# Kernel optimization log

Measured on AMD Instinct MI355X. Metric: run time of the kernel, lower is better.

The kernel has to match this reference:

```python
import jax, jax.numpy as jnp
import numpy as np

N = 50000      # nodes
E = 800000     # message edges
P = 200000     # prediction edges
C_IN = 64      # in_channels
C_H = 64       # hidden_channels


def setup_inputs() -> dict:
    key = jax.random.key(0)
    ks = jax.random.split(key, 20)
    s = 0.05
    inp = {
        "x": jax.random.normal(ks[0], (N, C_IN), jnp.float32),
        "prediction_edges": jax.random.randint(ks[1], (2, P), 0, N, dtype=jnp.int32),
        "message_edges": jax.random.randint(ks[2], (2, E), 0, N, dtype=jnp.int32),
        "message_edgewt": jax.random.uniform(ks[3], (E,), jnp.float32),
        # conv1 params
        "coef1": jnp.float32(0.5),
        "pool1_w": jax.random.normal(ks[4], (C_IN, C_IN), jnp.float32) * s,
        "pool1_b": jnp.zeros((C_IN,), jnp.float32),
        "fin1_w": jax.random.normal(ks[5], (C_H, 2 * C_IN), jnp.float32) * s,
        "fin1_b": jnp.zeros((C_H,), jnp.float32),
        # conv2 params
        "coef2": jnp.float32(0.5),
        "pool2_w": jax.random.normal(ks[6], (C_H, C_H), jnp.float32) * s,
        "pool2_b": jnp.zeros((C_H,), jnp.float32),
        "fin2_w": jax.random.normal(ks[7], (C_H, 2 * C_H), jnp.float32) * s,
        "fin2_b": jnp.zeros((C_H,), jnp.float32),
        # edge heads
        "ewp_w": jax.random.normal(ks[8], (1, 2 * C_H), jnp.float32) * s,
        "ewp_b": jnp.zeros((1,), jnp.float32),
        "ep_w": jax.random.normal(ks[9], (1, 2 * C_H), jnp.float32) * s,
        "ep_b": jnp.zeros((1,), jnp.float32),
    }
    return inp


def _relu(v):
    return jnp.maximum(v, 0)


def _sage_conv(x, src, dst, ew, coef, pw, pb, fw, fb):
    n = x.shape[0]
    all_src = jnp.concatenate([src, dst])   # [2E]
    all_dst = jnp.concatenate([dst, src])   # [2E]
    neigh = x[all_src]                       # [2E, C] gather
    w2 = jnp.concatenate([ew, ew])           # [2E]
    edge_feat = neigh * (1.0 + coef * w2[:, None])
    pooled = _relu(edge_feat @ pw.T + pb)    # [2E, C]
    # self-loop edges (src == dst) routed to dummy segment n
    seg = jnp.where(all_src != all_dst, all_dst, n)
    agg = jax.ops.segment_max(pooled, seg, num_segments=n + 1)[:n]
    agg = jnp.where(jnp.isfinite(agg), agg, 0.0)  # empty nodes -> 0
    h = jnp.concatenate([x, agg], axis=-1)   # [N, 2C]
    return _relu(h @ fw.T + fb)


def reference(x, prediction_edges, message_edges, message_edgewt,
              coef1, pool1_w, pool1_b, fin1_w, fin1_b,
              coef2, pool2_w, pool2_b, fin2_w, fin2_b,
              ewp_w, ewp_b, ep_w, ep_b):
    src, dst = message_edges[0], message_edges[1]
    h = _sage_conv(x, src, dst, message_edgewt, coef1, pool1_w, pool1_b, fin1_w, fin1_b)
    h = _sage_conv(h, src, dst, message_edgewt, coef2, pool2_w, pool2_b, fin2_w, fin2_b)
    emb = jnp.concatenate([h[prediction_edges[0]], h[prediction_edges[1]]], axis=-1)  # [P, 2C]
    edge_weights = _relu(emb @ ewp_w.T + ewp_b)   # [P, 1]
    edge_predictor = emb @ ep_w.T + ep_b          # [P, 1]
    return edge_weights, edge_predictor
```

## Files before the change

### kernel.cpp

```cpp
#include <hip/hip_runtime.h>


typedef _Float16 h16;
typedef __attribute__((ext_vector_type(4))) _Float16 h16x4;
typedef __attribute__((ext_vector_type(4))) float f32x4;
#define MFMA16(a, b, c) __builtin_amdgcn_mfma_f32_16x16x16f16(a, b, c, 0, 0, 0)

#define NBMAX 1600
#define NFB   128

__global__ void cvt_kernel(const float* __restrict__ X,
                           h16* __restrict__ X16, int n8) {
    int t = blockIdx.x * blockDim.x + threadIdx.x;
    const int stride = gridDim.x * blockDim.x;
    for (int i = t; i < n8; i += stride) {
        const float4 a = ((const float4*)X)[2 * i];
        const float4 b = ((const float4*)X)[2 * i + 1];
        h16x4 lo = {(h16)a.x, (h16)a.y, (h16)a.z, (h16)a.w};
        h16x4 hi = {(h16)b.x, (h16)b.y, (h16)b.z, (h16)b.w};
        ((h16x4*)X16)[2 * i] = lo;
        ((h16x4*)X16)[2 * i + 1] = hi;
    }
}

__global__ __launch_bounds__(256, 2)
void mmA_kernel(const h16* __restrict__ X16, const float* __restrict__ W,
                h16* __restrict__ Z, int ntiles) {
    const int lane = threadIdx.x & 63;
    const int c = lane & 15, q = lane >> 4;
    int wave = (int)((blockIdx.x * blockDim.x + threadIdx.x) >> 6);
    const int nwaves = (int)((gridDim.x * blockDim.x) >> 6);
    h16x4 bf[4][4];
#pragma unroll
    for (int ct = 0; ct < 4; ++ct)
#pragma unroll
        for (int ks = 0; ks < 4; ++ks) {
            const float4 w4 = *(const float4*)(W + (ct * 16 + c) * 64 + ks * 16 + q * 4);
            bf[ct][ks] = (h16x4){(h16)w4.x, (h16)w4.y, (h16)w4.z, (h16)w4.w};
        }
    for (int t = wave; t < ntiles; t += nwaves) {
        const int n0 = t * 16;
        const h16* __restrict__ xrow = X16 + (size_t)(n0 + c) * 64 + q * 4;
        h16x4 af[4];
#pragma unroll
        for (int ks = 0; ks < 4; ++ks) af[ks] = *(const h16x4*)(xrow + ks * 16);
        f32x4 acc[4];
#pragma unroll
        for (int ct = 0; ct < 4; ++ct) acc[ct] = (f32x4){0.f, 0.f, 0.f, 0.f};
#pragma unroll
        for (int ct = 0; ct < 4; ++ct)
#pragma unroll
            for (int ks = 0; ks < 4; ++ks)
                acc[ct] = MFMA16(af[ks], bf[ct][ks], acc[ct]);
#pragma unroll
        for (int ct = 0; ct < 4; ++ct)
#pragma unroll
            for (int m = 0; m < 4; ++m)
                Z[(size_t)(n0 + q * 4 + m) * 64 + ct * 16 + c] = (h16)acc[ct][m];
    }
}

__global__ __launch_bounds__(256, 2)
void finA_kernel(const h16* __restrict__ XA, const h16* __restrict__ XB,
                 const float* __restrict__ W, const float* __restrict__ b,
                 h16* __restrict__ H, int ntiles) {
    const int lane = threadIdx.x & 63;
    const int c = lane & 15, q = lane >> 4;
    int wave = (int)((blockIdx.x * blockDim.x + threadIdx.x) >> 6);
    const int nwaves = (int)((gridDim.x * blockDim.x) >> 6);
    h16x4 bf[4][8];
#pragma unroll
    for (int ct = 0; ct < 4; ++ct)
#pragma unroll
        for (int ks = 0; ks < 8; ++ks) {
            const float4 w4 = *(const float4*)(W + (ct * 16 + c) * 128 + ks * 16 + q * 4);
            bf[ct][ks] = (h16x4){(h16)w4.x, (h16)w4.y, (h16)w4.z, (h16)w4.w};
        }
    float bc[4];
#pragma unroll
    for (int ct = 0; ct < 4; ++ct) bc[ct] = b[ct * 16 + c];
    for (int t = wave; t < ntiles; t += nwaves) {
        const int n0 = t * 16;
        const h16* __restrict__ ra = XA + (size_t)(n0 + c) * 64 + q * 4;
        const h16* __restrict__ rb = XB + (size_t)(n0 + c) * 64 + q * 4;
        h16x4 af[8];
#pragma unroll
        for (int ks = 0; ks < 4; ++ks) {
            af[ks] = *(const h16x4*)(ra + ks * 16);
            af[4 + ks] = *(const h16x4*)(rb + ks * 16);
        }
        f32x4 acc[4];
#pragma unroll
        for (int ct = 0; ct < 4; ++ct) acc[ct] = (f32x4){bc[ct], bc[ct], bc[ct], bc[ct]};
#pragma unroll
        for (int ct = 0; ct < 4; ++ct)
#pragma unroll
            for (int ks = 0; ks < 8; ++ks)
                acc[ct] = MFMA16(af[ks], bf[ct][ks], acc[ct]);
#pragma unroll
        for (int ct = 0; ct < 4; ++ct)
#pragma unroll
            for (int m = 0; m < 4; ++m)
                H[(size_t)(n0 + q * 4 + m) * 64 + ct * 16 + c] =
                    (h16)fmaxf(acc[ct][m], 0.f);
    }
}

__global__ __launch_bounds__(256, 2)
void fin2A_kernel(const h16* __restrict__ XA, const h16* __restrict__ XB,
                  const float* __restrict__ W, const float* __restrict__ b,
                  const float* __restrict__ ewp_w, const float* __restrict__ ep_w,
                  float4* __restrict__ nodeheads, int ntiles) {
    const int lane = threadIdx.x & 63;
    const int c = lane & 15, q = lane >> 4;
    int wave = (int)((blockIdx.x * blockDim.x + threadIdx.x) >> 6);
    const int nwaves = (int)((gridDim.x * blockDim.x) >> 6);
    h16x4 bf[4][8];
#pragma unroll
    for (int ct = 0; ct < 4; ++ct)
#pragma unroll
        for (int ks = 0; ks < 8; ++ks) {
            const float4 w4 = *(const float4*)(W + (ct * 16 + c) * 128 + ks * 16 + q * 4);
            bf[ct][ks] = (h16x4){(h16)w4.x, (h16)w4.y, (h16)w4.z, (h16)w4.w};
        }
    float bc[4], hw1s[4], hw1d[4], hw2s[4], hw2d[4];
#pragma unroll
    for (int ct = 0; ct < 4; ++ct) {
        bc[ct] = b[ct * 16 + c];
        hw1s[ct] = ewp_w[ct * 16 + c];
        hw1d[ct] = ewp_w[64 + ct * 16 + c];
        hw2s[ct] = ep_w[ct * 16 + c];
        hw2d[ct] = ep_w[64 + ct * 16 + c];
    }
    for (int t = wave; t < ntiles; t += nwaves) {
        const int n0 = t * 16;
        const h16* __restrict__ ra = XA + (size_t)(n0 + c) * 64 + q * 4;
        const h16* __restrict__ rb = XB + (size_t)(n0 + c) * 64 + q * 4;
        h16x4 af[8];
#pragma unroll
        for (int ks = 0; ks < 4; ++ks) {
            af[ks] = *(const h16x4*)(ra + ks * 16);
            af[4 + ks] = *(const h16x4*)(rb + ks * 16);
        }
        f32x4 acc[4];
#pragma unroll
        for (int ct = 0; ct < 4; ++ct) acc[ct] = (f32x4){bc[ct], bc[ct], bc[ct], bc[ct]};
#pragma unroll
        for (int ct = 0; ct < 4; ++ct)
#pragma unroll
            for (int ks = 0; ks < 8; ++ks)
                acc[ct] = MFMA16(af[ks], bf[ct][ks], acc[ct]);
        f32x4 r1 = {0.f, 0.f, 0.f, 0.f}, r2 = r1, r3 = r1, r4 = r1;
#pragma unroll
        for (int ct = 0; ct < 4; ++ct)
#pragma unroll
            for (int m = 0; m < 4; ++m) {
                const float h = fmaxf(acc[ct][m], 0.f);
                r1[m] = fmaf(hw1s[ct], h, r1[m]);
                r2[m] = fmaf(hw1d[ct], h, r2[m]);
                r3[m] = fmaf(hw2s[ct], h, r3[m]);
                r4[m] = fmaf(hw2d[ct], h, r4[m]);
            }
#pragma unroll
        for (int off = 1; off < 16; off <<= 1)
#pragma unroll
            for (int m = 0; m < 4; ++m) {
                r1[m] += __shfl_xor(r1[m], off, 16);
                r2[m] += __shfl_xor(r2[m], off, 16);
                r3[m] += __shfl_xor(r3[m], off, 16);
                r4[m] += __shfl_xor(r4[m], off, 16);
            }
        if (c == 0) {
#pragma unroll
            for (int m = 0; m < 4; ++m)
                nodeheads[n0 + q * 4 + m] =
                    make_float4(r1[m], r2[m], r3[m], r4[m]);
        }
    }
}

__global__ void hist_kernel(const int* __restrict__ esrc,
                            const int* __restrict__ edst,
                            int* __restrict__ bucketTotal,
                            int* __restrict__ blockBase, int E, int NB) {
    __shared__ int cnt[NBMAX];
    for (int b = threadIdx.x; b < NB; b += blockDim.x) cnt[b] = 0;
    __syncthreads();
    const int chunk = (E + gridDim.x - 1) / gridDim.x;
    const int start = blockIdx.x * chunk;
    const int end = min(start + chunk, E);
    for (int e = start + (int)threadIdx.x; e < end; e += blockDim.x) {
        const int s = esrc[e];
        const int d = edst[e];
        if (s != d) {
            atomicAdd(&cnt[d >> 5], 1);
            atomicAdd(&cnt[s >> 5], 1);
        }
    }
    __syncthreads();
    for (int b = threadIdx.x; b < NB; b += blockDim.x)
        blockBase[(size_t)blockIdx.x * NB + b] = atomicAdd(&bucketTotal[b], cnt[b]);
}

__global__ void scan_kernel(const int* __restrict__ deg,
                            int* __restrict__ offs, int n) {
    __shared__ int wsum[16];
    __shared__ int s_carry;
    const int tid = threadIdx.x;
    const int lane = tid & 63;
    const int wid = tid >> 6;
    if (tid == 0) s_carry = 0;
    __syncthreads();
    for (int base = 0; base < n; base += 1024) {
        const int i = base + tid;
        const int v = (i < n) ? deg[i] : 0;
        int x = v;
#pragma unroll
        for (int off = 1; off < 64; off <<= 1) {
            int t = __shfl_up(x, off, 64);
            if (lane >= off) x += t;
        }
        if (lane == 63) wsum[wid] = x;
        __syncthreads();
        if (wid == 0) {
            int wv = (lane < 16) ? wsum[lane] : 0;
#pragma unroll
            for (int off = 1; off < 16; off <<= 1) {
                int t = __shfl_up(wv, off, 64);
                if (lane >= off) wv += t;
            }
            if (lane < 16) wsum[lane] = wv;
        }
        __syncthreads();
        const int carry = s_carry;
        const int waveoff = (wid > 0) ? wsum[wid - 1] : 0;
        if (i < n) offs[i] = carry + waveoff + x - v;
        __syncthreads();
        if (tid == 0) s_carry = carry + wsum[15];
        __syncthreads();
    }
}

__global__ void binfill_kernel(const int* __restrict__ esrc,
                               const int* __restrict__ edst,
                               const float* __restrict__ ewt,
                               const int* __restrict__ bucketStart,
                               const int* __restrict__ blockBase,
                               unsigned* __restrict__ entries, int E, int NB) {
    __shared__ int cur[NBMAX];
    for (int b = threadIdx.x; b < NB; b += blockDim.x)
        cur[b] = bucketStart[b] + blockBase[(size_t)blockIdx.x * NB + b];
    __syncthreads();
    const int chunk = (E + gridDim.x - 1) / gridDim.x;
    const int start = blockIdx.x * chunk;
    const int end = min(start + chunk, E);
    for (int e = start + (int)threadIdx.x; e < end; e += blockDim.x) {
        const int s = esrc[e];
        const int d = edst[e];
        if (s != d) {
            const unsigned wq =
                (unsigned)fminf(ewt[e] * 2048.f + 0.5f, 2047.f) << 21;
            const int pd = atomicAdd(&cur[d >> 5], 1);
            entries[pd] = (unsigned)s | ((unsigned)(d & 31) << 16) | wq;
            const int ps = atomicAdd(&cur[s >> 5], 1);
            entries[ps] = (unsigned)d | ((unsigned)(s & 31) << 16) | wq;
        }
    }
}

__global__ void sortbucket_kernel(const int* __restrict__ bucketStart,
                                  const int* __restrict__ bucketTotal,
                                  const unsigned* __restrict__ in,
                                  unsigned* __restrict__ out,
                                  int* __restrict__ nodeBeg, int n, int NB) {
    __shared__ int bin[32];
    __shared__ int cur[32];
    const int bkt = blockIdx.x;
    const int beg = bucketStart[bkt];
    const int cnt = bucketTotal[bkt];
    if (threadIdx.x < 32) bin[threadIdx.x] = 0;
    __syncthreads();
    for (int i = threadIdx.x; i < cnt; i += blockDim.x)
        atomicAdd(&bin[(in[beg + i] >> 16) & 31u], 1);
    __syncthreads();
    if (threadIdx.x == 0) {
        int run = 0;
#pragma unroll
        for (int r = 0; r < 32; ++r) { cur[r] = run; run += bin[r]; }
    }
    __syncthreads();
    if (threadIdx.x < 32) {
        const int node = bkt * 32 + (int)threadIdx.x;
        if (node < n) nodeBeg[node] = beg + cur[threadIdx.x];
    }
    if (bkt == NB - 1 && threadIdx.x == 0) nodeBeg[n] = beg + cnt;
    __syncthreads();
    for (int i = threadIdx.x; i < cnt; i += blockDim.x) {
        const unsigned e = in[beg + i];
        const int pos = beg + atomicAdd(&cur[(e >> 16) & 31u], 1);
        out[pos] = e;
    }
}

__global__ void aggregateN_kernel(const int* __restrict__ nodeBeg,
                                  const unsigned* __restrict__ entries,
                                  const h16* __restrict__ Z,
                                  const float* __restrict__ pb,
                                  const float* __restrict__ coefp,
                                  h16* __restrict__ agg, int n) {
    const int lane = threadIdx.x & 63;
    int wave = (int)((blockIdx.x * blockDim.x + threadIdx.x) >> 6);
    const int nwaves = (int)((gridDim.x * blockDim.x) >> 6);
    const float coefq = coefp[0] * (1.f / 2048.f);
    const float pbc = pb[lane];
    for (int d = wave; d < n; d += nwaves) {
        const int du = __builtin_amdgcn_readfirstlane(d);
        const int beg = nodeBeg[du];
        const int end = nodeBeg[du + 1];
        float m0 = 0.f, m1 = 0.f, m2 = 0.f, m3 = 0.f;
        int i = beg;
        for (; i + 4 <= end; i += 4) {
            const unsigned e0 = (unsigned)__builtin_amdgcn_readfirstlane((int)entries[i]);
            const unsigned e1 = (unsigned)__builtin_amdgcn_readfirstlane((int)entries[i + 1]);
            const unsigned e2 = (unsigned)__builtin_amdgcn_readfirstlane((int)entries[i + 2]);
            const unsigned e3 = (unsigned)__builtin_amdgcn_readfirstlane((int)entries[i + 3]);
            const float z0 = (float)Z[(size_t)(e0 & 0xffffu) * 64 + lane];
            const float z1 = (float)Z[(size_t)(e1 & 0xffffu) * 64 + lane];
            const float z2 = (float)Z[(size_t)(e2 & 0xffffu) * 64 + lane];
            const float z3 = (float)Z[(size_t)(e3 & 0xffffu) * 64 + lane];
            m0 = fmaxf(m0, fmaf(fmaf(coefq, (float)(e0 >> 21), 1.f), z0, pbc));
            m1 = fmaxf(m1, fmaf(fmaf(coefq, (float)(e1 >> 21), 1.f), z1, pbc));
            m2 = fmaxf(m2, fmaf(fmaf(coefq, (float)(e2 >> 21), 1.f), z2, pbc));
            m3 = fmaxf(m3, fmaf(fmaf(coefq, (float)(e3 >> 21), 1.f), z3, pbc));
        }
        for (; i < end; ++i) {
            const unsigned e = (unsigned)__builtin_amdgcn_readfirstlane((int)entries[i]);
            const float zv = (float)Z[(size_t)(e & 0xffffu) * 64 + lane];
            m0 = fmaxf(m0, fmaf(fmaf(coefq, (float)(e >> 21), 1.f), zv, pbc));
        }
        agg[(size_t)du * 64 + lane] = (h16)fmaxf(fmaxf(m0, m1), fmaxf(m2, m3));
    }
}

__global__ void headsP_kernel(const int* __restrict__ psrc,
                              const int* __restrict__ pdst,
                              const float4* __restrict__ nodeheads,
                              const float* __restrict__ ewp_b,
                              const float* __restrict__ ep_b,
                              float* __restrict__ out, int P) {
    int t = blockIdx.x * blockDim.x + threadIdx.x;
    const int stride = gridDim.x * blockDim.x;
    const float b1 = ewp_b[0], b2 = ep_b[0];
    for (; t < P; t += stride) {
        const float4 qs = nodeheads[psrc[t]];
        const float4 qd = nodeheads[pdst[t]];
        out[t] = fmaxf(qs.x + qd.y + b1, 0.f);
        out[(size_t)P + t] = qs.z + qd.w + b2;
    }
}

extern "C" void kernel_launch(void* const* d_in, const int* in_sizes, int n_in,
                              void* d_out, int out_size, void* d_ws, size_t ws_size,
                              hipStream_t stream) {
    const float* x      = (const float*)d_in[0];
    const int*   pe     = (const int*)d_in[1];
    const int*   me     = (const int*)d_in[2];
    const float* mew    = (const float*)d_in[3];
    const float* coef1  = (const float*)d_in[4];
    const float* p1w    = (const float*)d_in[5];
    const float* p1b    = (const float*)d_in[6];
    const float* f1w    = (const float*)d_in[7];
    const float* f1b    = (const float*)d_in[8];
    const float* coef2  = (const float*)d_in[9];
    const float* p2w    = (const float*)d_in[10];
    const float* p2b    = (const float*)d_in[11];
    const float* f2w    = (const float*)d_in[12];
    const float* f2b    = (const float*)d_in[13];
    const float* ewp_w  = (const float*)d_in[14];
    const float* ewp_b  = (const float*)d_in[15];
    const float* ep_w   = (const float*)d_in[16];
    const float* ep_b   = (const float*)d_in[17];

    const int n = in_sizes[0] / 64;
    const int P = in_sizes[1] / 2;
    const int E = in_sizes[2] / 2;
    const int NB = (n + 31) >> 5;
    const int ntiles = (n + 15) >> 4;

    float4* nodeheads = (float4*)d_ws;
    h16* z16   = (h16*)(nodeheads + n);
    h16* agg16 = z16 + (size_t)n * 64;
    h16* h1    = agg16 + (size_t)n * 64;
    h16* x16   = h1 + (size_t)n * 64;
    unsigned* entriesA = (unsigned*)(x16 + (size_t)n * 64);
    unsigned* entriesB = entriesA + 2 * (size_t)E;
    int* bucketTotal = (int*)(entriesB + 2 * (size_t)E);
    int* bucketStart = bucketTotal + NBMAX;
    int* nodeBeg     = bucketStart + NBMAX;
    int* blockBase   = nodeBeg + (n + 1);

    const int* esrc = me;
    const int* edst = me + E;
    const int* psrc = pe;
    const int* pdst = pe + P;

    const dim3 blk(256);
    const int mfGrid = (ntiles + 3) / 4;
    const int agGrid = 2048;
    const int hpGrid = (P + 255) / 256;

    cvt_kernel<<<1024, blk, 0, stream>>>(x, x16, n * 64 / 8);
    hipMemsetAsync(bucketTotal, 0, (size_t)NB * sizeof(int), stream);
    hist_kernel<<<NFB, blk, 0, stream>>>(esrc, edst, bucketTotal, blockBase, E, NB);
    scan_kernel<<<1, 1024, 0, stream>>>(bucketTotal, bucketStart, NB);
    binfill_kernel<<<NFB, blk, 0, stream>>>(esrc, edst, mew, bucketStart,
                                            blockBase, entriesA, E, NB);
    sortbucket_kernel<<<NB, blk, 0, stream>>>(bucketStart, bucketTotal,
                                              entriesA, entriesB, nodeBeg, n, NB);

    mmA_kernel<<<mfGrid, blk, 0, stream>>>(x16, p1w, z16, ntiles);
    aggregateN_kernel<<<agGrid, blk, 0, stream>>>(nodeBeg, entriesB, z16,
                                                  p1b, coef1, agg16, n);
    finA_kernel<<<mfGrid, blk, 0, stream>>>(x16, agg16, f1w, f1b, h1, ntiles);

    mmA_kernel<<<mfGrid, blk, 0, stream>>>(h1, p2w, z16, ntiles);
    aggregateN_kernel<<<agGrid, blk, 0, stream>>>(nodeBeg, entriesB, z16,
                                                  p2b, coef2, agg16, n);
    fin2A_kernel<<<mfGrid, blk, 0, stream>>>(h1, agg16, f2w, f2b,
                                             ewp_w, ep_w, nodeheads, ntiles);

    headsP_kernel<<<hpGrid, blk, 0, stream>>>(psrc, pdst, nodeheads,
                                              ewp_b, ep_b, (float*)d_out, P);
}
```

Baseline: 206.7 us.

## Fuse graph build into cooperative kernel and aggregation with final linear

Merges the histogram, scan, bin-fill and bucket-sort kernels into one cooperative kernel separated by grid syncs. It also fuses neighbour max-aggregation with the final linear layer per 32-node group, staging aggregates in LDS instead of writing them to global memory. The fp32-to-fp16 conversion pass is folded into the first matmul. The aim is fewer launches and less intermediate memory traffic, at the cost of grid-sync overhead and a fixed 32-node block granularity for aggregation.

```diff
diff --git a/kernel.cpp b/kernel.cpp
--- a/kernel.cpp
+++ b/kernel.cpp
@@ -1,4 +1,7 @@
 #include <hip/hip_runtime.h>
+#include <hip/hip_cooperative_groups.h>
+
+namespace cg = cooperative_groups;
 
 
 typedef _Float16 h16;
@@ -7,183 +10,25 @@
 #define MFMA16(a, b, c) __builtin_amdgcn_mfma_f32_16x16x16f16(a, b, c, 0, 0, 0)
 
 #define NBMAX 1600
-#define NFB   128
-
-__global__ void cvt_kernel(const float* __restrict__ X,
-                           h16* __restrict__ X16, int n8) {
-    int t = blockIdx.x * blockDim.x + threadIdx.x;
-    const int stride = gridDim.x * blockDim.x;
-    for (int i = t; i < n8; i += stride) {
-        const float4 a = ((const float4*)X)[2 * i];
-        const float4 b = ((const float4*)X)[2 * i + 1];
-        h16x4 lo = {(h16)a.x, (h16)a.y, (h16)a.z, (h16)a.w};
-        h16x4 hi = {(h16)b.x, (h16)b.y, (h16)b.z, (h16)b.w};
-        ((h16x4*)X16)[2 * i] = lo;
-        ((h16x4*)X16)[2 * i + 1] = hi;
-    }
-}
-
-__global__ __launch_bounds__(256, 2)
-void mmA_kernel(const h16* __restrict__ X16, const float* __restrict__ W,
-                h16* __restrict__ Z, int ntiles) {
-    const int lane = threadIdx.x & 63;
-    const int c = lane & 15, q = lane >> 4;
-    int wave = (int)((blockIdx.x * blockDim.x + threadIdx.x) >> 6);
-    const int nwaves = (int)((gridDim.x * blockDim.x) >> 6);
-    h16x4 bf[4][4];
-#pragma unroll
-    for (int ct = 0; ct < 4; ++ct)
-#pragma unroll
-        for (int ks = 0; ks < 4; ++ks) {
-            const float4 w4 = *(const float4*)(W + (ct * 16 + c) * 64 + ks * 16 + q * 4);
-            bf[ct][ks] = (h16x4){(h16)w4.x, (h16)w4.y, (h16)w4.z, (h16)w4.w};
-        }
-    for (int t = wave; t < ntiles; t += nwaves) {
-        const int n0 = t * 16;
-        const h16* __restrict__ xrow = X16 + (size_t)(n0 + c) * 64 + q * 4;
-        h16x4 af[4];
-#pragma unroll
-        for (int ks = 0; ks < 4; ++ks) af[ks] = *(const h16x4*)(xrow + ks * 16);
-        f32x4 acc[4];
-#pragma unroll
-        for (int ct = 0; ct < 4; ++ct) acc[ct] = (f32x4){0.f, 0.f, 0.f, 0.f};
-#pragma unroll
-        for (int ct = 0; ct < 4; ++ct)
-#pragma unroll
-            for (int ks = 0; ks < 4; ++ks)
-                acc[ct] = MFMA16(af[ks], bf[ct][ks], acc[ct]);
-#pragma unroll
-        for (int ct = 0; ct < 4; ++ct)
-#pragma unroll
-            for (int m = 0; m < 4; ++m)
-                Z[(size_t)(n0 + q * 4 + m) * 64 + ct * 16 + c] = (h16)acc[ct][m];
-    }
-}
-
-__global__ __launch_bounds__(256, 2)
-void finA_kernel(const h16* __restrict__ XA, const h16* __restrict__ XB,
-                 const float* __restrict__ W, const float* __restrict__ b,
-                 h16* __restrict__ H, int ntiles) {
-    const int lane = threadIdx.x & 63;
-    const int c = lane & 15, q = lane >> 4;
-    int wave = (int)((blockIdx.x * blockDim.x + threadIdx.x) >> 6);
-    const int nwaves = (int)((gridDim.x * blockDim.x) >> 6);
-    h16x4 bf[4][8];
-#pragma unroll
-    for (int ct = 0; ct < 4; ++ct)
-#pragma unroll
-        for (int ks = 0; ks < 8; ++ks) {
-            const float4 w4 = *(const float4*)(W + (ct * 16 + c) * 128 + ks * 16 + q * 4);
-            bf[ct][ks] = (h16x4){(h16)w4.x, (h16)w4.y, (h16)w4.z, (h16)w4.w};
-        }
-    float bc[4];
-#pragma unroll
-    for (int ct = 0; ct < 4; ++ct) bc[ct] = b[ct * 16 + c];
-    for (int t = wave; t < ntiles; t += nwaves) {
-        const int n0 = t * 16;
-        const h16* __restrict__ ra = XA + (size_t)(n0 + c) * 64 + q * 4;
-        const h16* __restrict__ rb = XB + (size_t)(n0 + c) * 64 + q * 4;
-        h16x4 af[8];
-#pragma unroll
-        for (int ks = 0; ks < 4; ++ks) {
-            af[ks] = *(const h16x4*)(ra + ks * 16);
-            af[4 + ks] = *(const h16x4*)(rb + ks * 16);
-        }
-        f32x4 acc[4];
-#pragma unroll
-        for (int ct = 0; ct < 4; ++ct) acc[ct] = (f32x4){bc[ct], bc[ct], bc[ct], bc[ct]};
-#pragma unroll
-        for (int ct = 0; ct < 4; ++ct)
-#pragma unroll
-            for (int ks = 0; ks < 8; ++ks)
-                acc[ct] = MFMA16(af[ks], bf[ct][ks], acc[ct]);
-#pragma unroll
-        for (int ct = 0; ct < 4; ++ct)
-#pragma unroll
-            for (int m = 0; m < 4; ++m)
-                H[(size_t)(n0 + q * 4 + m) * 64 + ct * 16 + c] =
-                    (h16)fmaxf(acc[ct][m], 0.f);
-    }
-}
-
-__global__ __launch_bounds__(256, 2)
-void fin2A_kernel(const h16* __restrict__ XA, const h16* __restrict__ XB,
-                  const float* __restrict__ W, const float* __restrict__ b,
-                  const float* __restrict__ ewp_w, const float* __restrict__ ep_w,
-                  float4* __restrict__ nodeheads, int ntiles) {
-    const int lane = threadIdx.x & 63;
-    const int c = lane & 15, q = lane >> 4;
-    int wave = (int)((blockIdx.x * blockDim.x + threadIdx.x) >> 6);
-    const int nwaves = (int)((gridDim.x * blockDim.x) >> 6);
-    h16x4 bf[4][8];
-#pragma unroll
-    for (int ct = 0; ct < 4; ++ct)
-#pragma unroll
-        for (int ks = 0; ks < 8; ++ks) {
-            const float4 w4 = *(const float4*)(W + (ct * 16 + c) * 128 + ks * 16 + q * 4);
-            bf[ct][ks] = (h16x4){(h16)w4.x, (h16)w4.y, (h16)w4.z, (h16)w4.w};
-        }
-    float bc[4], hw1s[4], hw1d[4], hw2s[4], hw2d[4];
-#pragma unroll
-    for (int ct = 0; ct < 4; ++ct) {
-        bc[ct] = b[ct * 16 + c];
-        hw1s[ct] = ewp_w[ct * 16 + c];
-        hw1d[ct] = ewp_w[64 + ct * 16 + c];
-        hw2s[ct] = ep_w[ct * 16 + c];
-        hw2d[ct] = ep_w[64 + ct * 16 + c];
-    }
-    for (int t = wave; t < ntiles; t += nwaves) {
-        const int n0 = t * 16;
-        const h16* __restrict__ ra = XA + (size_t)(n0 + c) * 64 + q * 4;
-        const h16* __restrict__ rb = XB + (size_t)(n0 + c) * 64 + q * 4;
-        h16x4 af[8];
-#pragma unroll
-        for (int ks = 0; ks < 4; ++ks) {
-            af[ks] = *(const h16x4*)(ra + ks * 16);
-            af[4 + ks] = *(const h16x4*)(rb + ks * 16);
-        }
-        f32x4 acc[4];
-#pragma unroll
-        for (int ct = 0; ct < 4; ++ct) acc[ct] = (f32x4){bc[ct], bc[ct], bc[ct], bc[ct]};
-#pragma unroll
-        for (int ct = 0; ct < 4; ++ct)
-#pragma unroll
-            for (int ks = 0; ks < 8; ++ks)
-                acc[ct] = MFMA16(af[ks], bf[ct][ks], acc[ct]);
-        f32x4 r1 = {0.f, 0.f, 0.f, 0.f}, r2 = r1, r3 = r1, r4 = r1;
-#pragma unroll
-        for (int ct = 0; ct < 4; ++ct)
-#pragma unroll
-            for (int m = 0; m < 4; ++m) {
-                const float h = fmaxf(acc[ct][m], 0.f);
-                r1[m] = fmaf(hw1s[ct], h, r1[m]);
-                r2[m] = fmaf(hw1d[ct], h, r2[m]);
-                r3[m] = fmaf(hw2s[ct], h, r3[m]);
-                r4[m] = fmaf(hw2d[ct], h, r4[m]);
-            }
-#pragma unroll
-        for (int off = 1; off < 16; off <<= 1)
-#pragma unroll
-            for (int m = 0; m < 4; ++m) {
-                r1[m] += __shfl_xor(r1[m], off, 16);
-                r2[m] += __shfl_xor(r2[m], off, 16);
-                r3[m] += __shfl_xor(r3[m], off, 16);
-                r4[m] += __shfl_xor(r4[m], off, 16);
-            }
-        if (c == 0) {
-#pragma unroll
-            for (int m = 0; m < 4; ++m)
-                nodeheads[n0 + q * 4 + m] =
-                    make_float4(r1[m], r2[m], r3[m], r4[m]);
-        }
-    }
-}
-
-__global__ void hist_kernel(const int* __restrict__ esrc,
-                            const int* __restrict__ edst,
-                            int* __restrict__ bucketTotal,
-                            int* __restrict__ blockBase, int E, int NB) {
+#define NFBC  256
+
+__global__ void coopbuild_kernel(const int* __restrict__ esrc,
+                                 const int* __restrict__ edst,
+                                 const float* __restrict__ ewt,
+                                 int* __restrict__ bucketTotal,
+                                 int* __restrict__ bucketStart,
+                                 int* __restrict__ blockBase,
+                                 unsigned* __restrict__ entriesA,
+                                 unsigned* __restrict__ entriesB,
+                                 int* __restrict__ nodeBeg,
+                                 int E, int NB, int n) {
+    cg::grid_group grid = cg::this_grid();
     __shared__ int cnt[NBMAX];
+    __shared__ int wsum[4];
+    __shared__ int s_carry;
+    __shared__ int bin[32];
+    __shared__ int cur32[32];
+
     for (int b = threadIdx.x; b < NB; b += blockDim.x) cnt[b] = 0;
     __syncthreads();
     const int chunk = (E + gridDim.x - 1) / gridDim.x;
@@ -200,145 +45,300 @@
     __syncthreads();
     for (int b = threadIdx.x; b < NB; b += blockDim.x)
         blockBase[(size_t)blockIdx.x * NB + b] = atomicAdd(&bucketTotal[b], cnt[b]);
-}
-
-__global__ void scan_kernel(const int* __restrict__ deg,
-                            int* __restrict__ offs, int n) {
-    __shared__ int wsum[16];
-    __shared__ int s_carry;
-    const int tid = threadIdx.x;
-    const int lane = tid & 63;
-    const int wid = tid >> 6;
-    if (tid == 0) s_carry = 0;
+    grid.sync();
+
+    if (blockIdx.x == 0) {
+        const int tid = threadIdx.x;
+        const int lane = tid & 63;
+        const int wid = tid >> 6;
+        if (tid == 0) s_carry = 0;
+        __syncthreads();
+        for (int base = 0; base < NB; base += blockDim.x) {
+            const int i = base + tid;
+            const int v = (i < NB) ? bucketTotal[i] : 0;
+            int x = v;
+#pragma unroll
+            for (int off = 1; off < 64; off <<= 1) {
+                int t = __shfl_up(x, off, 64);
+                if (lane >= off) x += t;
+            }
+            if (lane == 63) wsum[wid] = x;
+            __syncthreads();
+            if (wid == 0 && lane < 4) {
+                int wv = wsum[lane];
+#pragma unroll
+                for (int off = 1; off < 4; off <<= 1) {
+                    int t = __shfl_up(wv, off, 64);
+                    if (lane >= off) wv += t;
+                }
+                wsum[lane] = wv;
+            }
+            __syncthreads();
+            const int carry = s_carry;
+            const int waveoff = (wid > 0) ? wsum[wid - 1] : 0;
+            if (i < NB) bucketStart[i] = carry + waveoff + x - v;
+            __syncthreads();
+            if (tid == 0) s_carry = carry + wsum[3];
+            __syncthreads();
+        }
+    }
+    grid.sync();
+
+    for (int b = threadIdx.x; b < NB; b += blockDim.x)
+        cnt[b] = bucketStart[b] + blockBase[(size_t)blockIdx.x * NB + b];
     __syncthreads();
-    for (int base = 0; base < n; base += 1024) {
-        const int i = base + tid;
-        const int v = (i < n) ? deg[i] : 0;
-        int x = v;
-#pragma unroll
-        for (int off = 1; off < 64; off <<= 1) {
-            int t = __shfl_up(x, off, 64);
-            if (lane >= off) x += t;
-        }
-        if (lane == 63) wsum[wid] = x;
-        __syncthreads();
-        if (wid == 0) {
-            int wv = (lane < 16) ? wsum[lane] : 0;
-#pragma unroll
-            for (int off = 1; off < 16; off <<= 1) {
-                int t = __shfl_up(wv, off, 64);
-                if (lane >= off) wv += t;
-            }
-            if (lane < 16) wsum[lane] = wv;
-        }
-        __syncthreads();
-        const int carry = s_carry;
-        const int waveoff = (wid > 0) ? wsum[wid - 1] : 0;
-        if (i < n) offs[i] = carry + waveoff + x - v;
-        __syncthreads();
-        if (tid == 0) s_carry = carry + wsum[15];
-        __syncthreads();
-    }
-}
-
-__global__ void binfill_kernel(const int* __restrict__ esrc,
-                               const int* __restrict__ edst,
-                               const float* __restrict__ ewt,
-                               const int* __restrict__ bucketStart,
-                               const int* __restrict__ blockBase,
-                               unsigned* __restrict__ entries, int E, int NB) {
-    __shared__ int cur[NBMAX];
-    for (int b = threadIdx.x; b < NB; b += blockDim.x)
-        cur[b] = bucketStart[b] + blockBase[(size_t)blockIdx.x * NB + b];
-    __syncthreads();
-    const int chunk = (E + gridDim.x - 1) / gridDim.x;
-    const int start = blockIdx.x * chunk;
-    const int end = min(start + chunk, E);
     for (int e = start + (int)threadIdx.x; e < end; e += blockDim.x) {
         const int s = esrc[e];
         const int d = edst[e];
         if (s != d) {
             const unsigned wq =
                 (unsigned)fminf(ewt[e] * 2048.f + 0.5f, 2047.f) << 21;
-            const int pd = atomicAdd(&cur[d >> 5], 1);
-            entries[pd] = (unsigned)s | ((unsigned)(d & 31) << 16) | wq;
-            const int ps = atomicAdd(&cur[s >> 5], 1);
-            entries[ps] = (unsigned)d | ((unsigned)(s & 31) << 16) | wq;
-        }
+            const int pd = atomicAdd(&cnt[d >> 5], 1);
+            entriesA[pd] = (unsigned)s | ((unsigned)(d & 31) << 16) | wq;
+            const int ps = atomicAdd(&cnt[s >> 5], 1);
+            entriesA[ps] = (unsigned)d | ((unsigned)(s & 31) << 16) | wq;
+        }
+    }
+    grid.sync();
+
+    for (int bkt = blockIdx.x; bkt < NB; bkt += gridDim.x) {
+        const int beg = bucketStart[bkt];
+        const int cn = bucketTotal[bkt];
+        if (threadIdx.x < 32) bin[threadIdx.x] = 0;
+        __syncthreads();
+        for (int i = threadIdx.x; i < cn; i += blockDim.x)
+            atomicAdd(&bin[(entriesA[beg + i] >> 16) & 31u], 1);
+        __syncthreads();
+        if (threadIdx.x == 0) {
+            int run = 0;
+#pragma unroll
+            for (int r = 0; r < 32; ++r) { cur32[r] = run; run += bin[r]; }
+        }
+        __syncthreads();
+        if (threadIdx.x < 32) {
+            const int node = bkt * 32 + (int)threadIdx.x;
+            if (node < n) nodeBeg[node] = beg + cur32[threadIdx.x];
+        }
+        if (bkt == NB - 1 && threadIdx.x == 0) nodeBeg[n] = beg + cn;
+        __syncthreads();
+        for (int i = threadIdx.x; i < cn; i += blockDim.x) {
+            const unsigned e = entriesA[beg + i];
+            const int pos = beg + atomicAdd(&cur32[(e >> 16) & 31u], 1);
+            entriesB[pos] = e;
+        }
+        __syncthreads();
     }
 }
 
-__global__ void sortbucket_kernel(const int* __restrict__ bucketStart,
-                                  const int* __restrict__ bucketTotal,
-                                  const unsigned* __restrict__ in,
-                                  unsigned* __restrict__ out,
-                                  int* __restrict__ nodeBeg, int n, int NB) {
-    __shared__ int bin[32];
-    __shared__ int cur[32];
-    const int bkt = blockIdx.x;
-    const int beg = bucketStart[bkt];
-    const int cnt = bucketTotal[bkt];
-    if (threadIdx.x < 32) bin[threadIdx.x] = 0;
-    __syncthreads();
-    for (int i = threadIdx.x; i < cnt; i += blockDim.x)
-        atomicAdd(&bin[(in[beg + i] >> 16) & 31u], 1);
-    __syncthreads();
-    if (threadIdx.x == 0) {
-        int run = 0;
-#pragma unroll
-        for (int r = 0; r < 32; ++r) { cur[r] = run; run += bin[r]; }
-    }
-    __syncthreads();
-    if (threadIdx.x < 32) {
-        const int node = bkt * 32 + (int)threadIdx.x;
-        if (node < n) nodeBeg[node] = beg + cur[threadIdx.x];
-    }
-    if (bkt == NB - 1 && threadIdx.x == 0) nodeBeg[n] = beg + cnt;
-    __syncthreads();
-    for (int i = threadIdx.x; i < cnt; i += blockDim.x) {
-        const unsigned e = in[beg + i];
-        const int pos = beg + atomicAdd(&cur[(e >> 16) & 31u], 1);
-        out[pos] = e;
-    }
-}
-
-__global__ void aggregateN_kernel(const int* __restrict__ nodeBeg,
-                                  const unsigned* __restrict__ entries,
-                                  const h16* __restrict__ Z,
-                                  const float* __restrict__ pb,
-                                  const float* __restrict__ coefp,
-                                  h16* __restrict__ agg, int n) {
+template <bool XFP32>
+__global__ __launch_bounds__(256, 2)
+void mmA_kernel(const void* __restrict__ Xv, const float* __restrict__ W,
+                h16* __restrict__ Z, int ntiles) {
     const int lane = threadIdx.x & 63;
+    const int c = lane & 15, q = lane >> 4;
     int wave = (int)((blockIdx.x * blockDim.x + threadIdx.x) >> 6);
     const int nwaves = (int)((gridDim.x * blockDim.x) >> 6);
-    const float coefq = coefp[0] * (1.f / 2048.f);
-    const float pbc = pb[lane];
-    for (int d = wave; d < n; d += nwaves) {
-        const int du = __builtin_amdgcn_readfirstlane(d);
-        const int beg = nodeBeg[du];
-        const int end = nodeBeg[du + 1];
-        float m0 = 0.f, m1 = 0.f, m2 = 0.f, m3 = 0.f;
-        int i = beg;
-        for (; i + 4 <= end; i += 4) {
-            const unsigned e0 = (unsigned)__builtin_amdgcn_readfirstlane((int)entries[i]);
-            const unsigned e1 = (unsigned)__builtin_amdgcn_readfirstlane((int)entries[i + 1]);
-            const unsigned e2 = (unsigned)__builtin_amdgcn_readfirstlane((int)entries[i + 2]);
-            const unsigned e3 = (unsigned)__builtin_amdgcn_readfirstlane((int)entries[i + 3]);
-            const float z0 = (float)Z[(size_t)(e0 & 0xffffu) * 64 + lane];
-            const float z1 = (float)Z[(size_t)(e1 & 0xffffu) * 64 + lane];
-            const float z2 = (float)Z[(size_t)(e2 & 0xffffu) * 64 + lane];
-            const float z3 = (float)Z[(size_t)(e3 & 0xffffu) * 64 + lane];
-            m0 = fmaxf(m0, fmaf(fmaf(coefq, (float)(e0 >> 21), 1.f), z0, pbc));
-            m1 = fmaxf(m1, fmaf(fmaf(coefq, (float)(e1 >> 21), 1.f), z1, pbc));
-            m2 = fmaxf(m2, fmaf(fmaf(coefq, (float)(e2 >> 21), 1.f), z2, pbc));
-            m3 = fmaxf(m3, fmaf(fmaf(coefq, (float)(e3 >> 21), 1.f), z3, pbc));
-        }
-        for (; i < end; ++i) {
-            const unsigned e = (unsigned)__builtin_amdgcn_readfirstlane((int)entries[i]);
-            const float zv = (float)Z[(size_t)(e & 0xffffu) * 64 + lane];
-            m0 = fmaxf(m0, fmaf(fmaf(coefq, (float)(e >> 21), 1.f), zv, pbc));
-        }
-        agg[(size_t)du * 64 + lane] = (h16)fmaxf(fmaxf(m0, m1), fmaxf(m2, m3));
+    h16x4 bf[4][4];
+#pragma unroll
+    for (int ct = 0; ct < 4; ++ct)
+#pragma unroll
+        for (int ks = 0; ks < 4; ++ks) {
+            const float4 w4 = *(const float4*)(W + (ct * 16 + c) * 64 + ks * 16 + q * 4);
+            bf[ct][ks] = (h16x4){(h16)w4.x, (h16)w4.y, (h16)w4.z, (h16)w4.w};
+        }
+    for (int t = wave; t < ntiles; t += nwaves) {
+        const int n0 = t * 16;
+        h16x4 af[4];
+        if constexpr (XFP32) {
+            const float* xr = (const float*)Xv + (size_t)(n0 + c) * 64 + q * 4;
+#pragma unroll
+            for (int ks = 0; ks < 4; ++ks) {
+                const float4 v = *(const float4*)(xr + ks * 16);
+                af[ks] = (h16x4){(h16)v.x, (h16)v.y, (h16)v.z, (h16)v.w};
+            }
+        } else {
+            const h16* xr = (const h16*)Xv + (size_t)(n0 + c) * 64 + q * 4;
+#pragma unroll
+            for (int ks = 0; ks < 4; ++ks) af[ks] = *(const h16x4*)(xr + ks * 16);
+        }
+        f32x4 acc[4];
+#pragma unroll
+        for (int ct = 0; ct < 4; ++ct) acc[ct] = (f32x4){0.f, 0.f, 0.f, 0.f};
+#pragma unroll
+        for (int ct = 0; ct < 4; ++ct)
+#pragma unroll
+            for (int ks = 0; ks < 4; ++ks)
+                acc[ct] = MFMA16(af[ks], bf[ct][ks], acc[ct]);
+#pragma unroll
+        for (int ct = 0; ct < 4; ++ct)
+#pragma unroll
+            for (int m = 0; m < 4; ++m)
+                Z[(size_t)(n0 + q * 4 + m) * 64 + ct * 16 + c] = (h16)acc[ct][m];
+    }
+}
+
+template <bool XFP32, bool HEADS>
+__global__ __launch_bounds__(256, 2)
+void aggfin_kernel(const int* __restrict__ nodeBeg,
+                   const unsigned* __restrict__ entries,
+                   const h16* __restrict__ Z,
+                   const float* __restrict__ pb,
+                   const float* __restrict__ coefp,
+                   const void* __restrict__ Xv,
+                   const float* __restrict__ W,
+                   const float* __restrict__ bvec,
+                   const float* __restrict__ ewp_w,
+                   const float* __restrict__ ep_w,
+                   h16* __restrict__ H,
+                   float4* __restrict__ nodeheads,
+                   int n) {
+    __shared__ h16 ldsA[32 * 64];
+    __shared__ float4 ldsR[2][16][2];
+    const int lane = threadIdx.x & 63;
+    const int wid = threadIdx.x >> 6;
+    const int g0 = blockIdx.x * 32;
+
+    {
+        const float coefq = coefp[0] * (1.f / 2048.f);
+        const float pbc = pb[lane];
+        for (int ln = wid; ln < 32; ln += 4) {
+            const int node = g0 + ln;
+            float m0 = 0.f, m1 = 0.f, m2 = 0.f, m3 = 0.f;
+            if (node < n) {
+                const int beg = nodeBeg[node];
+                const int end = nodeBeg[node + 1];
+                int i = beg;
+                for (; i + 4 <= end; i += 4) {
+                    const unsigned e0 = (unsigned)__builtin_amdgcn_readfirstlane((int)entries[i]);
+                    const unsigned e1 = (unsigned)__builtin_amdgcn_readfirstlane((int)entries[i + 1]);
+                    const unsigned e2 = (unsigned)__builtin_amdgcn_readfirstlane((int)entries[i + 2]);
+                    const unsigned e3 = (unsigned)__builtin_amdgcn_readfirstlane((int)entries[i + 3]);
+                    const float z0 = (float)Z[(size_t)(e0 & 0xffffu) * 64 + lane];
+                    const float z1 = (float)Z[(size_t)(e1 & 0xffffu) * 64 + lane];
+                    const float z2 = (float)Z[(size_t)(e2 & 0xffffu) * 64 + lane];
+                    const float z3 = (float)Z[(size_t)(e3 & 0xffffu) * 64 + lane];
+                    m0 = fmaxf(m0, fmaf(fmaf(coefq, (float)(e0 >> 21), 1.f), z0, pbc));
+                    m1 = fmaxf(m1, fmaf(fmaf(coefq, (float)(e1 >> 21), 1.f), z1, pbc));
+                    m2 = fmaxf(m2, fmaf(fmaf(coefq, (float)(e2 >> 21), 1.f), z2, pbc));
+                    m3 = fmaxf(m3, fmaf(fmaf(coefq, (float)(e3 >> 21), 1.f), z3, pbc));
+                }
+                for (; i < end; ++i) {
+                    const unsigned e = (unsigned)__builtin_amdgcn_readfirstlane((int)entries[i]);
+                    const float zv = (float)Z[(size_t)(e & 0xffffu) * 64 + lane];
+                    m0 = fmaxf(m0, fmaf(fmaf(coefq, (float)(e >> 21), 1.f), zv, pbc));
+                }
+            }
+            const float m = fmaxf(fmaxf(m0, m1), fmaxf(m2, m3));
+            ldsA[ln * 64 + ((((lane >> 2) ^ ln) & 15) << 2) + (lane & 3)] = (h16)m;
+        }
+    }
+    __syncthreads();
+
+    {
+        const int t = wid & 1;
+        const int p = wid >> 1;
+        const int c = lane & 15, q = lane >> 4;
+        const int n0 = g0 + t * 16;
+        h16x4 bf[2][8];
+        float bc[2], hw1s[2], hw1d[2], hw2s[2], hw2d[2];
+#pragma unroll
+        for (int cc = 0; cc < 2; ++cc) {
+            const int ct = p * 2 + cc;
+#pragma unroll
+            for (int ks = 0; ks < 8; ++ks) {
+                const float4 w4 = *(const float4*)(W + (ct * 16 + c) * 128 + ks * 16 + q * 4);
+                bf[cc][ks] = (h16x4){(h16)w4.x, (h16)w4.y, (h16)w4.z, (h16)w4.w};
+            }
+            bc[cc] = bvec[ct * 16 + c];
+            if constexpr (HEADS) {
+                hw1s[cc] = ewp_w[ct * 16 + c];
+                hw1d[cc] = ewp_w[64 + ct * 16 + c];
+                hw2s[cc] = ep_w[ct * 16 + c];
+                hw2d[cc] = ep_w[64 + ct * 16 + c];
+            }
+        }
+        const int arow = n0 + c;
+        const bool rv = (arow < n);
+        h16x4 af[8];
+        const h16x4 zero4 = {(h16)0.f, (h16)0.f, (h16)0.f, (h16)0.f};
+        if constexpr (XFP32) {
+            const float* xr = (const float*)Xv + (size_t)arow * 64 + q * 4;
+#pragma unroll
+            for (int ks = 0; ks < 4; ++ks) {
+                if (rv) {
+                    const float4 v = *(const float4*)(xr + ks * 16);
+                    af[ks] = (h16x4){(h16)v.x, (h16)v.y, (h16)v.z, (h16)v.w};
+                } else af[ks] = zero4;
+            }
+        } else {
+            const h16* xr = (const h16*)Xv + (size_t)arow * 64 + q * 4;
+#pragma unroll
+            for (int ks = 0; ks < 4; ++ks)
+                af[ks] = rv ? *(const h16x4*)(xr + ks * 16) : zero4;
+        }
+#pragma unroll
+        for (int ks = 0; ks < 4; ++ks)
+            af[4 + ks] = *(const h16x4*)&ldsA[(t * 16 + c) * 64 +
+                                             ((((ks * 4 + q) ^ c) & 15) << 2)];
+        f32x4 acc[2];
+#pragma unroll
+        for (int cc = 0; cc < 2; ++cc) acc[cc] = (f32x4){bc[cc], bc[cc], bc[cc], bc[cc]};
+#pragma unroll
+        for (int cc = 0; cc < 2; ++cc)
+#pragma unroll
+            for (int ks = 0; ks < 8; ++ks)
+                acc[cc] = MFMA16(af[ks], bf[cc][ks], acc[cc]);
+        if constexpr (!HEADS) {
+#pragma unroll
+            for (int cc = 0; cc < 2; ++cc) {
+                const int ct = p * 2 + cc;
+#pragma unroll
+                for (int m = 0; m < 4; ++m) {
+                    const int row = n0 + q * 4 + m;
+                    if (row < n)
+                        H[(size_t)row * 64 + ct * 16 + c] = (h16)fmaxf(acc[cc][m], 0.f);
+                }
+            }
+        } else {
+            f32x4 r1 = {0.f, 0.f, 0.f, 0.f}, r2 = r1, r3 = r1, r4 = r1;
+#pragma unroll
+            for (int cc = 0; cc < 2; ++cc)
+#pragma unroll
+                for (int m = 0; m < 4; ++m) {
+                    const float h = fmaxf(acc[cc][m], 0.f);
+                    r1[m] = fmaf(hw1s[cc], h, r1[m]);
+                    r2[m] = fmaf(hw1d[cc], h, r2[m]);
+                    r3[m] = fmaf(hw2s[cc], h, r3[m]);
+                    r4[m] = fmaf(hw2d[cc], h, r4[m]);
+                }
+#pragma unroll
+            for (int off = 1; off < 16; off <<= 1)
+#pragma unroll
+                for (int m = 0; m < 4; ++m) {
+                    r1[m] += __shfl_xor(r1[m], off, 16);
+                    r2[m] += __shfl_xor(r2[m], off, 16);
+                    r3[m] += __shfl_xor(r3[m], off, 16);
+                    r4[m] += __shfl_xor(r4[m], off, 16);
+                }
+            if (c == 0) {
+#pragma unroll
+                for (int m = 0; m < 4; ++m)
+                    ldsR[t][q * 4 + m][p] = make_float4(r1[m], r2[m], r3[m], r4[m]);
+            }
+        }
+    }
+    if constexpr (HEADS) {
+        __syncthreads();
+        const int tid = threadIdx.x;
+        if (tid < 32) {
+            const int node = g0 + tid;
+            if (node < n) {
+                const float4 a = ldsR[tid >> 4][tid & 15][0];
+                const float4 bq = ldsR[tid >> 4][tid & 15][1];
+                nodeheads[node] = make_float4(a.x + bq.x, a.y + bq.y,
+                                              a.z + bq.z, a.w + bq.w);
+            }
+        }
     }
 }
 
@@ -389,10 +389,8 @@
 
     float4* nodeheads = (float4*)d_ws;
     h16* z16   = (h16*)(nodeheads + n);
-    h16* agg16 = z16 + (size_t)n * 64;
-    h16* h1    = agg16 + (size_t)n * 64;
-    h16* x16   = h1 + (size_t)n * 64;
-    unsigned* entriesA = (unsigned*)(x16 + (size_t)n * 64);
+    h16* h1    = z16 + (size_t)n * 64;
+    unsigned* entriesA = (unsigned*)(h1 + (size_t)n * 64);
     unsigned* entriesB = entriesA + 2 * (size_t)E;
     int* bucketTotal = (int*)(entriesB + 2 * (size_t)E);
     int* bucketStart = bucketTotal + NBMAX;
@@ -406,28 +404,29 @@
 
     const dim3 blk(256);
     const int mfGrid = (ntiles + 3) / 4;
-    const int agGrid = 2048;
+    const int agGrid = NB;
     const int hpGrid = (P + 255) / 256;
 
-    cvt_kernel<<<1024, blk, 0, stream>>>(x, x16, n * 64 / 8);
     hipMemsetAsync(bucketTotal, 0, (size_t)NB * sizeof(int), stream);
-    hist_kernel<<<NFB, blk, 0, stream>>>(esrc, edst, bucketTotal, blockBase, E, NB);
-    scan_kernel<<<1, 1024, 0, stream>>>(bucketTotal, bucketStart, NB);
-    binfill_kernel<<<NFB, blk, 0, stream>>>(esrc, edst, mew, bucketStart,
-                                            blockBase, entriesA, E, NB);
-    sortbucket_kernel<<<NB, blk, 0, stream>>>(bucketStart, bucketTotal,
-                                              entriesA, entriesB, nodeBeg, n, NB);
-
-    mmA_kernel<<<mfGrid, blk, 0, stream>>>(x16, p1w, z16, ntiles);
-    aggregateN_kernel<<<agGrid, blk, 0, stream>>>(nodeBeg, entriesB, z16,
-                                                  p1b, coef1, agg16, n);
-    finA_kernel<<<mfGrid, blk, 0, stream>>>(x16, agg16, f1w, f1b, h1, ntiles);
-
-    mmA_kernel<<<mfGrid, blk, 0, stream>>>(h1, p2w, z16, ntiles);
-    aggregateN_kernel<<<agGrid, blk, 0, stream>>>(nodeBeg, entriesB, z16,
-                                                  p2b, coef2, agg16, n);
-    fin2A_kernel<<<mfGrid, blk, 0, stream>>>(h1, agg16, f2w, f2b,
-                                             ewp_w, ep_w, nodeheads, ntiles);
+    {
+        int E_ = E, NB_ = NB, n_ = n;
+        void* args[] = {(void*)&esrc, (void*)&edst, (void*)&mew,
+                        (void*)&bucketTotal, (void*)&bucketStart, (void*)&blockBase,
+                        (void*)&entriesA, (void*)&entriesB, (void*)&nodeBeg,
+                        (void*)&E_, (void*)&NB_, (void*)&n_};
+        hipLaunchCooperativeKernel((const void*)coopbuild_kernel,
+                                   dim3(NFBC), blk, args, 0, stream);
+    }
+
+    mmA_kernel<true><<<mfGrid, blk, 0, stream>>>(x, p1w, z16, ntiles);
+    aggfin_kernel<true, false><<<agGrid, blk, 0, stream>>>(
+        nodeBeg, entriesB, z16, p1b, coef1, x, f1w, f1b,
+        nullptr, nullptr, h1, nullptr, n);
+
+    mmA_kernel<false><<<mfGrid, blk, 0, stream>>>(h1, p2w, z16, ntiles);
+    aggfin_kernel<false, true><<<agGrid, blk, 0, stream>>>(
+        nodeBeg, entriesB, z16, p2b, coef2, h1, f2w, f2b,
+        ewp_w, ep_w, nullptr, nodeheads, n);
 
     headsP_kernel<<<hpGrid, blk, 0, stream>>>(psrc, pdst, nodeheads,
                                               ewp_b, ep_b, (float*)d_out, P);
```

After: 425.5 us. 2.06x slower.
